# Performance work log

Measured on AMD Instinct MI355X. Metric: run time of the kernel, lower is better.

The kernel has to match this reference:

```python
import jax, jax.numpy as jnp
import numpy as np
from jax import lax

B, F, T = 16, 128, 4000
N_RATES = 10
EPS = 1e-05


def setup_inputs() -> dict:
    key = jax.random.key(0)
    k_x, k_s = jax.random.split(key, 2)
    x = jax.random.uniform(k_x, (B, F, T), dtype=jnp.float32)
    means = jnp.array([0.61803, 0.3904, 0.1174, 0.0606, 0.0308,
                       0.0155, 0.0078, 0.0039, 0.002, 0.0001], dtype=jnp.float32)
    # s_k ~ Normal(mean, 0.01*mean); stored as log|s_k|, shape (10, F)
    noise = jax.random.normal(k_s, (N_RATES, F), dtype=jnp.float32)
    s_log = jnp.log(jnp.abs(means[:, None] * (1.0 + 0.01 * noise)))
    alpha_log = jnp.full((F,), jnp.log(jnp.float32(0.8)), dtype=jnp.float32)
    delta_log = jnp.full((F,), jnp.log(jnp.float32(10.0)), dtype=jnp.float32)
    r_log = jnp.full((F,), jnp.log(jnp.float32(0.25)), dtype=jnp.float32)
    return {"x": x, "s_log": s_log, "alpha_log": alpha_log,
            "delta_log": delta_log, "r_log": r_log}


def reference(x, s_log, alpha_log, delta_log, r_log):
    # x: (B, F, T); s_log: (10, F); alpha/delta/r_log: (F,)
    s = jnp.exp(s_log)                      # (10, F)
    alpha = jnp.exp(alpha_log)[:, None]     # (F, 1) -> broadcast over T
    delta = jnp.exp(delta_log)[:, None]
    r = jnp.exp(r_log)[:, None]
    eps = jnp.float32(EPS)

    s_b = s[:, None, :]                     # (10, 1, F)
    init = jnp.broadcast_to(x[..., 0], (N_RATES,) + x.shape[:-1])  # (10, B, F)

    def step(carry, xt):
        # carry: (10, B, F); xt: (B, F)
        carry = (1.0 - s_b) * carry + s_b * xt
        return carry, carry

    xt_seq = jnp.moveaxis(x, -1, 0)         # (T, B, F)
    _, sm = lax.scan(step, init, xt_seq[1:])  # (T-1, 10, B, F)
    smoother = jnp.concatenate([init[None], sm], axis=0)  # (T, 10, B, F)
    smoother = jnp.moveaxis(smoother, 0, -1)               # (10, B, F, T)

    # AGC in log domain: M^(-alpha) computed as exp(-alpha*(log eps + log1p(M/eps)))
    smooth = jnp.exp(-alpha * (jnp.log(eps) + jnp.log1p(smoother / eps)))
    pcen = (x[None] * smooth + delta) ** r - delta ** r    # (10, B, F, T)
    return jnp.transpose(pcen, (1, 0, 2, 3))               # (B, 10, F, T)
```

## Files before the change

### kernel.cpp

```cpp
#include <hip/hip_runtime.h>


constexpr int B_ = 16, F_ = 128, T_ = 4000, R_ = 10;
constexpr float EPS_ = 1e-5f;
constexpr int TPB = 256;
constexpr int WPB = TPB / 64;

__global__ __launch_bounds__(TPB) void pcen_kernel(
    const float* __restrict__ x,
    const float* __restrict__ s_log,
    const float* __restrict__ alpha_log,
    const float* __restrict__ delta_log,
    const float* __restrict__ r_log,
    float* __restrict__ out)
{
    const int wid  = blockIdx.x * WPB + (threadIdx.x >> 6);
    const int lane = threadIdx.x & 63;

    const int b    = wid / (F_ * R_);
    const int rem  = wid - b * (F_ * R_);
    const int f    = rem / R_;
    const int rate = rem - f * R_;

    const float s     = __builtin_expf(s_log[rate * F_ + f]);
    const float a     = 1.0f - s;
    const float alpha = __builtin_expf(alpha_log[f]);
    const float delta = __builtin_expf(delta_log[f]);
    const float r     = __builtin_expf(r_log[f]);
    const float delta_r = __builtin_exp2f(r * __builtin_log2f(delta));

    const float a2 = a * a, a3 = a2 * a, a4 = a2 * a2;
    const float a8 = a4 * a4, a16 = a8 * a8, a32 = a16 * a16;
    const float a64 = a32 * a32, a128 = a64 * a64;

    const float* xrow = x   + (size_t)(b * F_ + f) * T_;
    float*       orow = out + (size_t)((b * R_ + rate) * F_ + f) * T_;

    float carry = xrow[0];

    for (int t0 = 0; t0 < T_; t0 += 256) {
        const int t = t0 + lane * 4;
        float4 v = make_float4(0.f, 0.f, 0.f, 0.f);
        if (t < T_) v = *reinterpret_cast<const float4*>(xrow + t);

        const float l0 = s * v.x;
        const float l1 = fmaf(a, l0, s * v.y);
        const float l2 = fmaf(a, l1, s * v.z);
        const float l3 = fmaf(a, l2, s * v.w);

        float Y = l3;
        if (lane == 0) Y = fmaf(a4, carry, Y);

        float up;
        up = __shfl_up(Y, 1);  if (lane >= 1)  Y = fmaf(a4,   up, Y);
        up = __shfl_up(Y, 2);  if (lane >= 2)  Y = fmaf(a8,   up, Y);
        up = __shfl_up(Y, 4);  if (lane >= 4)  Y = fmaf(a16,  up, Y);
        up = __shfl_up(Y, 8);  if (lane >= 8)  Y = fmaf(a32,  up, Y);
        up = __shfl_up(Y, 16); if (lane >= 16) Y = fmaf(a64,  up, Y);
        up = __shfl_up(Y, 32); if (lane >= 32) Y = fmaf(a128, up, Y);

        float yin = __shfl_up(Y, 1);
        if (lane == 0) yin = carry;
        carry = __shfl(Y, 63);

        const float m0 = fmaf(a,  yin, l0);
        const float m1 = fmaf(a2, yin, l1);
        const float m2 = fmaf(a3, yin, l2);
        const float m3 = fmaf(a4, yin, l3);

        if (t < T_) {
            float4 o;
            {
                const float sm = __builtin_exp2f(-alpha * __builtin_log2f(EPS_ + m0));
                o.x = __builtin_exp2f(r * __builtin_log2f(fmaf(v.x, sm, delta))) - delta_r;
            }
            {
                const float sm = __builtin_exp2f(-alpha * __builtin_log2f(EPS_ + m1));
                o.y = __builtin_exp2f(r * __builtin_log2f(fmaf(v.y, sm, delta))) - delta_r;
            }
            {
                const float sm = __builtin_exp2f(-alpha * __builtin_log2f(EPS_ + m2));
                o.z = __builtin_exp2f(r * __builtin_log2f(fmaf(v.z, sm, delta))) - delta_r;
            }
            {
                const float sm = __builtin_exp2f(-alpha * __builtin_log2f(EPS_ + m3));
                o.w = __builtin_exp2f(r * __builtin_log2f(fmaf(v.w, sm, delta))) - delta_r;
            }
            *reinterpret_cast<float4*>(orow + t) = o;
        }
    }
}

extern "C" void kernel_launch(void* const* d_in, const int* in_sizes, int n_in,
                              void* d_out, int out_size, void* d_ws, size_t ws_size,
                              hipStream_t stream) {
    const float* x         = (const float*)d_in[0];
    const float* s_log     = (const float*)d_in[1];
    const float* alpha_log = (const float*)d_in[2];
    const float* delta_log = (const float*)d_in[3];
    const float* r_log     = (const float*)d_in[4];
    float* out = (float*)d_out;

    const int n_waves = B_ * F_ * R_;
    const int blocks  = n_waves / WPB;
    pcen_kernel<<<blocks, TPB, 0, stream>>>(x, s_log, alpha_log, delta_log, r_log, out);
}
```

Baseline: 105.9 us.

## Process eight elements per lane, reorder wave mapping, use nontemporal stores

Each lane now handles 8 consecutive time samples per iteration instead of 4. This halves the number of loop iterations and the shuffle-based scan passes over the 4000-length row. Wave indexing is changed so consecutive waves share the same rate and walk over f, which alters the x reuse pattern across concurrent waves. Outputs are written with nontemporal stores to avoid polluting cache with write-once data. The trade-offs are higher register pressure and more idle lanes on the final partial chunk.

```diff
diff --git a/kernel.cpp b/kernel.cpp
--- a/kernel.cpp
+++ b/kernel.cpp
@@ -1,5 +1,7 @@
 #include <hip/hip_runtime.h>
 
+
+typedef float f32x4 __attribute__((ext_vector_type(4)));
 
 constexpr int B_ = 16, F_ = 128, T_ = 4000, R_ = 10;
 constexpr float EPS_ = 1e-5f;
@@ -17,10 +19,10 @@
     const int wid  = blockIdx.x * WPB + (threadIdx.x >> 6);
     const int lane = threadIdx.x & 63;
 
-    const int b    = wid / (F_ * R_);
-    const int rem  = wid - b * (F_ * R_);
-    const int f    = rem / R_;
-    const int rate = rem - f * R_;
+    const int b    = wid / (R_ * F_);
+    const int rem  = wid - b * (R_ * F_);
+    const int rate = rem / F_;
+    const int f    = rem - rate * F_;
 
     const float s     = __builtin_expf(s_log[rate * F_ + f]);
     const float a     = 1.0f - s;
@@ -29,64 +31,76 @@
     const float r     = __builtin_expf(r_log[f]);
     const float delta_r = __builtin_exp2f(r * __builtin_log2f(delta));
 
-    const float a2 = a * a, a3 = a2 * a, a4 = a2 * a2;
-    const float a8 = a4 * a4, a16 = a8 * a8, a32 = a16 * a16;
-    const float a64 = a32 * a32, a128 = a64 * a64;
+    const float a2 = a * a,     a3 = a2 * a,    a4 = a2 * a2;
+    const float a5 = a4 * a,    a6 = a4 * a2,   a7 = a4 * a3,   a8 = a4 * a4;
+    const float a16 = a8 * a8,  a32 = a16 * a16, a64 = a32 * a32;
+    const float a128 = a64 * a64, a256 = a128 * a128;
 
     const float* xrow = x   + (size_t)(b * F_ + f) * T_;
     float*       orow = out + (size_t)((b * R_ + rate) * F_ + f) * T_;
 
     float carry = xrow[0];
 
-    for (int t0 = 0; t0 < T_; t0 += 256) {
-        const int t = t0 + lane * 4;
-        float4 v = make_float4(0.f, 0.f, 0.f, 0.f);
-        if (t < T_) v = *reinterpret_cast<const float4*>(xrow + t);
+    auto pcen1 = [&](float xv, float m) -> float {
+        const float sm = __builtin_exp2f(-alpha * __builtin_log2f(EPS_ + m));
+        return __builtin_exp2f(r * __builtin_log2f(fmaf(xv, sm, delta))) - delta_r;
+    };
 
-        const float l0 = s * v.x;
-        const float l1 = fmaf(a, l0, s * v.y);
-        const float l2 = fmaf(a, l1, s * v.z);
-        const float l3 = fmaf(a, l2, s * v.w);
+    for (int t0 = 0; t0 < T_; t0 += 512) {
+        const int t = t0 + lane * 8;
+        const bool act = (t < T_);
+        float4 v0 = make_float4(0.f, 0.f, 0.f, 0.f);
+        float4 v1 = make_float4(0.f, 0.f, 0.f, 0.f);
+        if (act) {
+            v0 = *reinterpret_cast<const float4*>(xrow + t);
+            v1 = *reinterpret_cast<const float4*>(xrow + t + 4);
+        }
 
-        float Y = l3;
-        if (lane == 0) Y = fmaf(a4, carry, Y);
+        const float l0 = s * v0.x;
+        const float l1 = fmaf(a, l0, s * v0.y);
+        const float l2 = fmaf(a, l1, s * v0.z);
+        const float l3 = fmaf(a, l2, s * v0.w);
+        const float l4 = fmaf(a, l3, s * v1.x);
+        const float l5 = fmaf(a, l4, s * v1.y);
+        const float l6 = fmaf(a, l5, s * v1.z);
+        const float l7 = fmaf(a, l6, s * v1.w);
+
+        float Y = l7;
+        if (lane == 0) Y = fmaf(a8, carry, Y);
 
         float up;
-        up = __shfl_up(Y, 1);  if (lane >= 1)  Y = fmaf(a4,   up, Y);
-        up = __shfl_up(Y, 2);  if (lane >= 2)  Y = fmaf(a8,   up, Y);
-        up = __shfl_up(Y, 4);  if (lane >= 4)  Y = fmaf(a16,  up, Y);
-        up = __shfl_up(Y, 8);  if (lane >= 8)  Y = fmaf(a32,  up, Y);
-        up = __shfl_up(Y, 16); if (lane >= 16) Y = fmaf(a64,  up, Y);
-        up = __shfl_up(Y, 32); if (lane >= 32) Y = fmaf(a128, up, Y);
+        up = __shfl_up(Y, 1);  if (lane >= 1)  Y = fmaf(a8,   up, Y);
+        up = __shfl_up(Y, 2);  if (lane >= 2)  Y = fmaf(a16,  up, Y);
+        up = __shfl_up(Y, 4);  if (lane >= 4)  Y = fmaf(a32,  up, Y);
+        up = __shfl_up(Y, 8);  if (lane >= 8)  Y = fmaf(a64,  up, Y);
+        up = __shfl_up(Y, 16); if (lane >= 16) Y = fmaf(a128, up, Y);
+        up = __shfl_up(Y, 32); if (lane >= 32) Y = fmaf(a256, up, Y);
 
         float yin = __shfl_up(Y, 1);
         if (lane == 0) yin = carry;
         carry = __shfl(Y, 63);
 
-        const float m0 = fmaf(a,  yin, l0);
-        const float m1 = fmaf(a2, yin, l1);
-        const float m2 = fmaf(a3, yin, l2);
-        const float m3 = fmaf(a4, yin, l3);
+        if (act) {
+            const float m0 = fmaf(a,  yin, l0);
+            const float m1 = fmaf(a2, yin, l1);
+            const float m2 = fmaf(a3, yin, l2);
+            const float m3 = fmaf(a4, yin, l3);
+            const float m4 = fmaf(a5, yin, l4);
+            const float m5 = fmaf(a6, yin, l5);
+            const float m6 = fmaf(a7, yin, l6);
+            const float m7 = fmaf(a8, yin, l7);
 
-        if (t < T_) {
-            float4 o;
-            {
-                const float sm = __builtin_exp2f(-alpha * __builtin_log2f(EPS_ + m0));
-                o.x = __builtin_exp2f(r * __builtin_log2f(fmaf(v.x, sm, delta))) - delta_r;
-            }
-            {
-                const float sm = __builtin_exp2f(-alpha * __builtin_log2f(EPS_ + m1));
-                o.y = __builtin_exp2f(r * __builtin_log2f(fmaf(v.y, sm, delta))) - delta_r;
-            }
-            {
-                const float sm = __builtin_exp2f(-alpha * __builtin_log2f(EPS_ + m2));
-                o.z = __builtin_exp2f(r * __builtin_log2f(fmaf(v.z, sm, delta))) - delta_r;
-            }
-            {
-                const float sm = __builtin_exp2f(-alpha * __builtin_log2f(EPS_ + m3));
-                o.w = __builtin_exp2f(r * __builtin_log2f(fmaf(v.w, sm, delta))) - delta_r;
-            }
-            *reinterpret_cast<float4*>(orow + t) = o;
+            f32x4 o0, o1;
+            o0.x = pcen1(v0.x, m0);
+            o0.y = pcen1(v0.y, m1);
+            o0.z = pcen1(v0.z, m2);
+            o0.w = pcen1(v0.w, m3);
+            o1.x = pcen1(v1.x, m4);
+            o1.y = pcen1(v1.y, m5);
+            o1.z = pcen1(v1.z, m6);
+            o1.w = pcen1(v1.w, m7);
+            __builtin_nontemporal_store(o0, reinterpret_cast<f32x4*>(orow + t));
+            __builtin_nontemporal_store(o1, reinterpret_cast<f32x4*>(orow + t + 4));
         }
     }
 }
@@ -101,7 +115,7 @@
     const float* r_log     = (const float*)d_in[4];
     float* out = (float*)d_out;
 
-    const int n_waves = B_ * F_ * R_;
+    const int n_waves = B_ * R_ * F_;
     const int blocks  = n_waves / WPB;
     pcen_kernel<<<blocks, TPB, 0, stream>>>(x, s_log, alpha_log, delta_log, r_log, out);
 }
```

Result: faster. 90.84 us (-14.2%).

## Split each scan row across a block's four waves with shared-memory carry combine

Applied to the files above, without the earlier changes.

Instead of one wave serially scanning a whole 4000-step row in 16 chunks, each row now gets a block of four waves, each covering 1024 timesteps. Every wave holds four chunks in registers and scans them with interleaved shuffles. Per-wave totals are combined through shared memory after a barrier, and per-lane powers of the decay factor re-inject the incoming carry. Outputs use nontemporal stores. This shortens the serial dependency chain and raises memory-level parallelism, at the cost of a block-level sync and more registers per thread.

```diff
diff --git a/kernel.cpp b/kernel.cpp
--- a/kernel.cpp
+++ b/kernel.cpp
@@ -1,10 +1,11 @@
 #include <hip/hip_runtime.h>
 
+
+typedef float f32x4 __attribute__((ext_vector_type(4)));
 
 constexpr int B_ = 16, F_ = 128, T_ = 4000, R_ = 10;
 constexpr float EPS_ = 1e-5f;
 constexpr int TPB = 256;
-constexpr int WPB = TPB / 64;
 
 __global__ __launch_bounds__(TPB) void pcen_kernel(
     const float* __restrict__ x,
@@ -14,13 +15,16 @@
     const float* __restrict__ r_log,
     float* __restrict__ out)
 {
-    const int wid  = blockIdx.x * WPB + (threadIdx.x >> 6);
+    __shared__ float eloc[4];
+
+    const int bid  = blockIdx.x;
+    const int b    = bid / (R_ * F_);
+    const int rem  = bid - b * (R_ * F_);
+    const int rate = rem / F_;
+    const int f    = rem - rate * F_;
+
+    const int wv   = threadIdx.x >> 6;
     const int lane = threadIdx.x & 63;
-
-    const int b    = wid / (F_ * R_);
-    const int rem  = wid - b * (F_ * R_);
-    const int f    = rem / R_;
-    const int rate = rem - f * R_;
 
     const float s     = __builtin_expf(s_log[rate * F_ + f]);
     const float a     = 1.0f - s;
@@ -31,62 +35,95 @@
 
     const float a2 = a * a, a3 = a2 * a, a4 = a2 * a2;
     const float a8 = a4 * a4, a16 = a8 * a8, a32 = a16 * a16;
-    const float a64 = a32 * a32, a128 = a64 * a64;
+    const float a64 = a32 * a32, a128 = a64 * a64, a256 = a128 * a128;
+    const float a512 = a256 * a256, a1024 = a512 * a512;
+
+    float pl = 1.0f;
+    pl *= (lane & 1)  ? a4   : 1.0f;
+    pl *= (lane & 2)  ? a8   : 1.0f;
+    pl *= (lane & 4)  ? a16  : 1.0f;
+    pl *= (lane & 8)  ? a32  : 1.0f;
+    pl *= (lane & 16) ? a64  : 1.0f;
+    pl *= (lane & 32) ? a128 : 1.0f;
 
     const float* xrow = x   + (size_t)(b * F_ + f) * T_;
     float*       orow = out + (size_t)((b * R_ + rate) * F_ + f) * T_;
 
-    float carry = xrow[0];
+    const int base = wv * 1024;
 
-    for (int t0 = 0; t0 < T_; t0 += 256) {
-        const int t = t0 + lane * 4;
-        float4 v = make_float4(0.f, 0.f, 0.f, 0.f);
-        if (t < T_) v = *reinterpret_cast<const float4*>(xrow + t);
+    f32x4 v[4];
+    bool  act[4];
+#pragma unroll
+    for (int c = 0; c < 4; ++c) {
+        const int t = base + c * 256 + lane * 4;
+        act[c] = (t < T_);
+        f32x4 z = {0.f, 0.f, 0.f, 0.f};
+        v[c] = act[c] ? *reinterpret_cast<const f32x4*>(xrow + t) : z;
+    }
 
-        const float l0 = s * v.x;
-        const float l1 = fmaf(a, l0, s * v.y);
-        const float l2 = fmaf(a, l1, s * v.z);
-        const float l3 = fmaf(a, l2, s * v.w);
+    float l[4][4];
+#pragma unroll
+    for (int c = 0; c < 4; ++c) {
+        l[c][0] = s * v[c].x;
+        l[c][1] = fmaf(a, l[c][0], s * v[c].y);
+        l[c][2] = fmaf(a, l[c][1], s * v[c].z);
+        l[c][3] = fmaf(a, l[c][2], s * v[c].w);
+    }
 
-        float Y = l3;
-        if (lane == 0) Y = fmaf(a4, carry, Y);
+    float Y[4] = {l[0][3], l[1][3], l[2][3], l[3][3]};
+    const float mult[6] = {a4, a8, a16, a32, a64, a128};
+#pragma unroll
+    for (int i = 0; i < 6; ++i) {
+        const int d = 1 << i;
+        float up[4];
+#pragma unroll
+        for (int c = 0; c < 4; ++c) up[c] = __shfl_up(Y[c], d);
+        if (lane >= d) {
+#pragma unroll
+            for (int c = 0; c < 4; ++c) Y[c] = fmaf(mult[i], up[c], Y[c]);
+        }
+    }
 
-        float up;
-        up = __shfl_up(Y, 1);  if (lane >= 1)  Y = fmaf(a4,   up, Y);
-        up = __shfl_up(Y, 2);  if (lane >= 2)  Y = fmaf(a8,   up, Y);
-        up = __shfl_up(Y, 4);  if (lane >= 4)  Y = fmaf(a16,  up, Y);
-        up = __shfl_up(Y, 8);  if (lane >= 8)  Y = fmaf(a32,  up, Y);
-        up = __shfl_up(Y, 16); if (lane >= 16) Y = fmaf(a64,  up, Y);
-        up = __shfl_up(Y, 32); if (lane >= 32) Y = fmaf(a128, up, Y);
+    float X[4];
+#pragma unroll
+    for (int c = 0; c < 4; ++c) X[c] = __shfl(Y[c], 63);
+    const float El = fmaf(a256, fmaf(a256, fmaf(a256, X[0], X[1]), X[2]), X[3]);
+    if (lane == 0) eloc[wv] = El;
+    __syncthreads();
 
-        float yin = __shfl_up(Y, 1);
-        if (lane == 0) yin = carry;
-        carry = __shfl(Y, 63);
+    float in = xrow[0];
+#pragma unroll
+    for (int vv = 0; vv < 3; ++vv)
+        if (vv < wv) in = fmaf(a1024, in, eloc[vv]);
 
-        const float m0 = fmaf(a,  yin, l0);
-        const float m1 = fmaf(a2, yin, l1);
-        const float m2 = fmaf(a3, yin, l2);
-        const float m3 = fmaf(a4, yin, l3);
+    float cin[4];
+    cin[0] = in;
+    cin[1] = fmaf(a256, cin[0], X[0]);
+    cin[2] = fmaf(a256, cin[1], X[1]);
+    cin[3] = fmaf(a256, cin[2], X[2]);
 
-        if (t < T_) {
-            float4 o;
-            {
-                const float sm = __builtin_exp2f(-alpha * __builtin_log2f(EPS_ + m0));
-                o.x = __builtin_exp2f(r * __builtin_log2f(fmaf(v.x, sm, delta))) - delta_r;
-            }
-            {
-                const float sm = __builtin_exp2f(-alpha * __builtin_log2f(EPS_ + m1));
-                o.y = __builtin_exp2f(r * __builtin_log2f(fmaf(v.y, sm, delta))) - delta_r;
-            }
-            {
-                const float sm = __builtin_exp2f(-alpha * __builtin_log2f(EPS_ + m2));
-                o.z = __builtin_exp2f(r * __builtin_log2f(fmaf(v.z, sm, delta))) - delta_r;
-            }
-            {
-                const float sm = __builtin_exp2f(-alpha * __builtin_log2f(EPS_ + m3));
-                o.w = __builtin_exp2f(r * __builtin_log2f(fmaf(v.w, sm, delta))) - delta_r;
-            }
-            *reinterpret_cast<float4*>(orow + t) = o;
+    auto pcen1 = [&](float xv, float m) -> float {
+        const float sm = __builtin_exp2f(-alpha * __builtin_log2f(EPS_ + m));
+        return __builtin_exp2f(r * __builtin_log2f(fmaf(xv, sm, delta))) - delta_r;
+    };
+
+#pragma unroll
+    for (int c = 0; c < 4; ++c) {
+        float u = __shfl_up(Y[c], 1);
+        float yy = (lane == 0) ? 0.0f : u;
+        const float yin = fmaf(pl, cin[c], yy);
+        if (act[c]) {
+            const float m0 = fmaf(a,  yin, l[c][0]);
+            const float m1 = fmaf(a2, yin, l[c][1]);
+            const float m2 = fmaf(a3, yin, l[c][2]);
+            const float m3 = fmaf(a4, yin, l[c][3]);
+            f32x4 o;
+            o.x = pcen1(v[c].x, m0);
+            o.y = pcen1(v[c].y, m1);
+            o.z = pcen1(v[c].z, m2);
+            o.w = pcen1(v[c].w, m3);
+            const int t = base + c * 256 + lane * 4;
+            __builtin_nontemporal_store(o, reinterpret_cast<f32x4*>(orow + t));
         }
     }
 }
@@ -101,7 +138,6 @@
     const float* r_log     = (const float*)d_in[4];
     float* out = (float*)d_out;
 
-    const int n_waves = B_ * F_ * R_;
-    const int blocks  = n_waves / WPB;
+    const int blocks = B_ * R_ * F_;
     pcen_kernel<<<blocks, TPB, 0, stream>>>(x, s_log, alpha_log, delta_log, r_log, out);
 }
```

After: 99.04 us. 6.4% less time.
